# Optimization experiments

Hardware: AMD Instinct MI355X
Metric: run time of the kernel (lower is better)

## Reference

```python
import jax, jax.numpy as jnp
import numpy as np

EPS = 1e-12

def squash(s):
    # standard capsule squash: ||s||^2/(1+||s||^2) * s/||s||
    n2 = jnp.sum(s * s, axis=-1, keepdims=True)
    return n2 / (1.0 + n2) * s / jnp.sqrt(n2 + EPS)

def setup_inputs() -> dict:
    key = jax.random.key(0)
    k1, k2 = jax.random.split(key)
    B, O, I, DOUT, DIN = 64, 32, 2048, 16, 16
    u = jax.random.normal(k1, (B, I, DIN), dtype=jnp.float32)
    # TruncatedNormal(stddev=0.1) init for W
    W = 0.1 * jax.random.truncated_normal(k2, -2.0, 2.0, (1, O, I, DOUT, DIN), dtype=jnp.float32)
    bias = jnp.full((1, O, DOUT), 0.1, dtype=jnp.float32)
    return {"u": u, "W": W, "bias": bias}

def reference(u, W, bias):
    routing_iterations = 3
    O = W.shape[1]
    # u: [B, I, DIN], W: [1, O, I, DOUT, DIN]
    u_norm = jnp.linalg.norm(u, axis=-1)                     # [B, I]
    # u_hat[b,o,i,d] = sum_k W[0,o,i,d,k] * u[b,i,k]  (batched matmul instead of tile+mul+sum)
    u_hat = jnp.einsum('oidk,bik->boid', W[0], u)            # [B, O, I, DOUT]
    u_hat_norm = jnp.linalg.norm(u_hat, axis=-1, keepdims=True)   # [B, O, I, 1]
    new_u_hat_norm = jnp.minimum(u_hat_norm, u_norm[:, None, :, None])
    u_hat = u_hat / (u_hat_norm + EPS) * new_u_hat_norm

    B = u.shape[0]
    b_ij = jnp.zeros((B, O, u.shape[1], 1), dtype=u.dtype)
    t_const = jnp.float32(np.log(0.9 * (O - 1)) - np.log(1.0 - 0.9))
    v_j = None
    c_ij = None
    for r in range(routing_iterations):
        c_ij = jax.nn.softmax(b_ij, axis=1)                  # softmax over out capsules
        s_j = jnp.sum(c_ij * u_hat, axis=2) + bias           # [B, O, DOUT]
        v_j = squash(s_j)
        if r < routing_iterations - 1:
            # gamma-routing agreement: distance between prediction and output
            d = jnp.linalg.norm(v_j[:, :, None, :] - u_hat, axis=-1, keepdims=True)  # [B,O,I,1]
            d_o = jnp.mean(d)
            d_p = d_o * 0.5
            t = t_const / (d_p - d_o + 1e-12)
            b_ij = t * d
    return (v_j, c_ij)
```

## Files before the change

### kernel.cpp

```cpp
#include <hip/hip_runtime.h>
#include <hip/hip_bf16.h>
#include <math.h>

#define BB 64
#define OO 32
#define II 2048
#define DD 16
#define CAPS_EPS 1e-12f
#define T_CONST 5.6312118f

#define GX 128
#define TI 16

#define OFF_DSUM 0ULL
#define OFF_V     16ULL
#define OFF_UNORM 32784ULL
#define OFF_UBF   163856ULL
#define OFF_WB    1212432ULL
#define OFF_DD    9601040ULL
#define OFF_CB    13795344ULL
#define OFF_PART  17989648ULL

typedef __attribute__((ext_vector_type(8))) short bf16x8;
typedef __attribute__((ext_vector_type(4))) float f32x4;

union AU { bf16x8 v; unsigned short h[8]; uint4 u4; };

__device__ __forceinline__ unsigned short f2bf(float x) {
    __hip_bfloat16 h = __float2bfloat16(x);
    unsigned short s; __builtin_memcpy(&s, &h, 2); return s;
}

__global__ __launch_bounds__(256) void uprep_kernel(
    const float* __restrict__ u, float* __restrict__ ws)
{
    const int gid = blockIdx.x * 256 + threadIdx.x;
    if (gid < 2) ws[OFF_DSUM + gid] = 0.f;
    const int i = gid >> 6, b = gid & 63;

    const float4* up = reinterpret_cast<const float4*>(u + ((size_t)b * II + i) * DD);
    float4 t0 = up[0], t1 = up[1], t2 = up[2], t3 = up[3];
    float un2 = t0.x*t0.x + t0.y*t0.y + t0.z*t0.z + t0.w*t0.w
              + t1.x*t1.x + t1.y*t1.y + t1.z*t1.z + t1.w*t1.w
              + t2.x*t2.x + t2.y*t2.y + t2.z*t2.z + t2.w*t2.w
              + t3.x*t3.x + t3.y*t3.y + t3.z*t3.z + t3.w*t3.w;
    ws[OFF_UNORM + (size_t)i * 64 + b] = sqrtf(un2);

    AU a0, a1;
    a0.h[0]=f2bf(t0.x); a0.h[1]=f2bf(t0.y); a0.h[2]=f2bf(t0.z); a0.h[3]=f2bf(t0.w);
    a0.h[4]=f2bf(t1.x); a0.h[5]=f2bf(t1.y); a0.h[6]=f2bf(t1.z); a0.h[7]=f2bf(t1.w);
    a1.h[0]=f2bf(t2.x); a1.h[1]=f2bf(t2.y); a1.h[2]=f2bf(t2.z); a1.h[3]=f2bf(t2.w);
    a1.h[4]=f2bf(t3.x); a1.h[5]=f2bf(t3.y); a1.h[6]=f2bf(t3.z); a1.h[7]=f2bf(t3.w);
    unsigned short* ubf = (unsigned short*)(ws + OFF_UBF);
    uint4* dst = reinterpret_cast<uint4*>(ubf + ((size_t)i * 64 + b) * 16);
    dst[0] = a0.u4; dst[1] = a1.u4;
}

__global__ __launch_bounds__(256) void s0w_kernel(
    const float* __restrict__ W, float* __restrict__ ws)
{
    const int og   = blockIdx.y;
    const int wave = threadIdx.x >> 6;
    const int lane = threadIdx.x & 63;
    const int o    = og * 4 + wave;
    const int q    = lane >> 4;
    const int n    = lane & 15;

    unsigned short* Wb = (unsigned short*)(ws + OFF_WB);
    const unsigned short* ubf = (const unsigned short*)(ws + OFF_UBF);
    const float* unorm = ws + OFF_UNORM;
    float* part = ws + OFF_PART;

    f32x4 s_acc[4];
    #pragma unroll
    for (int g = 0; g < 4; ++g) s_acc[g] = (f32x4){0.f, 0.f, 0.f, 0.f};

    for (int ii = 0; ii < TI; ++ii) {
        const int i = blockIdx.x * TI + ii;

        AU au; au.u4 = make_uint4(0, 0, 0, 0);
        if (q < 2) {
            const float* wp = W + (((size_t)o * II + i) * 16 + n) * 16 + q * 8;
            float4 w0 = *(const float4*)(wp);
            float4 w1 = *(const float4*)(wp + 4);
            au.h[0]=f2bf(w0.x); au.h[1]=f2bf(w0.y); au.h[2]=f2bf(w0.z); au.h[3]=f2bf(w0.w);
            au.h[4]=f2bf(w1.x); au.h[5]=f2bf(w1.y); au.h[6]=f2bf(w1.z); au.h[7]=f2bf(w1.w);
            *reinterpret_cast<uint4*>(Wb + (((size_t)o * II + i) * 2 + q) * 128 + n * 8) = au.u4;
        }

        f32x4 d4[4];
        #pragma unroll
        for (int g = 0; g < 4; ++g) {
            AU bu;
            bu.u4 = *reinterpret_cast<const uint4*>(
                ubf + ((size_t)i * 64 + g * 16 + n) * 16 + (q & 1) * 8);
            d4[g] = __builtin_amdgcn_mfma_f32_16x16x32_bf16(
                au.v, bu.v, (f32x4){0.f, 0.f, 0.f, 0.f}, 0, 0, 0);
        }

        #pragma unroll
        for (int g = 0; g < 4; ++g) {
            float n2 = d4[g][0]*d4[g][0] + d4[g][1]*d4[g][1]
                     + d4[g][2]*d4[g][2] + d4[g][3]*d4[g][3];
            n2 += __shfl_xor(n2, 16);
            n2 += __shfl_xor(n2, 32);
            const float rawn = sqrtf(n2);
            const float un = unorm[(size_t)i * 64 + g * 16 + n];
            const float cs = (1.0f / 32.0f) * fminf(rawn, un) / (rawn + CAPS_EPS);
            s_acc[g][0] += cs * d4[g][0];
            s_acc[g][1] += cs * d4[g][1];
            s_acc[g][2] += cs * d4[g][2];
            s_acc[g][3] += cs * d4[g][3];
        }
    }

    #pragma unroll
    for (int g = 0; g < 4; ++g) {
        float4 v = make_float4(s_acc[g][0], s_acc[g][1], s_acc[g][2], s_acc[g][3]);
        *reinterpret_cast<float4*>(
            part + (((size_t)blockIdx.x * OO + o) * 64 + g * 16 + n) * 16 + q * 4) = v;
    }
}

template<int SLOT>
__global__ __launch_bounds__(256) void dpass_kernel(float* __restrict__ ws)
{
    const int og   = blockIdx.y;
    const int wave = threadIdx.x >> 6;
    const int lane = threadIdx.x & 63;
    const int o    = og * 4 + wave;
    const int q    = lane >> 4;
    const int n    = lane & 15;

    const unsigned short* Wb  = (const unsigned short*)(ws + OFF_WB);
    const unsigned short* ubf = (const unsigned short*)(ws + OFF_UBF);
    const float* unorm = ws + OFF_UNORM;
    const float* v_ws  = ws + OFF_V;
    float* dws = ws + OFF_DD;

    f32x4 vreg[4];
    #pragma unroll
    for (int g = 0; g < 4; ++g)
        vreg[g] = *reinterpret_cast<const f32x4*>(
            v_ws + ((size_t)(g * 16 + n) * OO + o) * 16 + q * 4);

    float dsum_local = 0.f;

    for (int ii = 0; ii < TI; ++ii) {
        const int i = blockIdx.x * TI + ii;

        AU au; au.u4 = make_uint4(0, 0, 0, 0);
        if (q < 2)
            au.u4 = *reinterpret_cast<const uint4*>(
                Wb + (((size_t)o * II + i) * 2 + q) * 128 + n * 8);

        f32x4 d4[4];
        #pragma unroll
        for (int g = 0; g < 4; ++g) {
            AU bu;
            bu.u4 = *reinterpret_cast<const uint4*>(
                ubf + ((size_t)i * 64 + g * 16 + n) * 16 + (q & 1) * 8);
            d4[g] = __builtin_amdgcn_mfma_f32_16x16x32_bf16(
                au.v, bu.v, (f32x4){0.f, 0.f, 0.f, 0.f}, 0, 0, 0);
        }

        #pragma unroll
        for (int g = 0; g < 4; ++g) {
            float n2 = d4[g][0]*d4[g][0] + d4[g][1]*d4[g][1]
                     + d4[g][2]*d4[g][2] + d4[g][3]*d4[g][3];
            n2 += __shfl_xor(n2, 16);
            n2 += __shfl_xor(n2, 32);
            const float rawn = sqrtf(n2);
            const float un = unorm[(size_t)i * 64 + g * 16 + n];
            const float scale = fminf(rawn, un) / (rawn + CAPS_EPS);
            float dd2 = 0.f;
            #pragma unroll
            for (int r = 0; r < 4; ++r) {
                float df = vreg[g][r] - scale * d4[g][r];
                dd2 += df * df;
            }
            dd2 += __shfl_xor(dd2, 16);
            dd2 += __shfl_xor(dd2, 32);
            const float dist = sqrtf(dd2);
            if (q == 0)
                dws[((size_t)i * OO + o) * 64 + g * 16 + n] = dist;
            dsum_local += (q == 0) ? dist : 0.f;
        }
    }

    #pragma unroll
    for (int off = 32; off > 0; off >>= 1)
        dsum_local += __shfl_down(dsum_local, off);
    __shared__ float red[4];
    if (lane == 0) red[wave] = dsum_local;
    __syncthreads();
    if (threadIdx.x == 0)
        atomicAdd(&ws[OFF_DSUM + SLOT], red[0] + red[1] + red[2] + red[3]);
}

template<int SLOT>
__global__ __launch_bounds__(256) void csoft_kernel(float* __restrict__ ws)
{
    const int wave = threadIdx.x >> 6;
    const int b    = threadIdx.x & 63;
    const int i    = blockIdx.x * 4 + wave;

    const float* dws = ws + OFF_DD;
    float* cb = ws + OFF_CB;
    const float dsum = ws[OFF_DSUM + SLOT];
    const float tval = T_CONST / (-0.5f * dsum * (1.0f / 4194304.0f) + 1e-12f);

    float dv[OO];
    #pragma unroll
    for (int o = 0; o < OO; ++o)
        dv[o] = tval * dws[((size_t)i * OO + o) * 64 + b];
    float m = -1e30f;
    #pragma unroll
    for (int o = 0; o < OO; ++o) m = fmaxf(m, dv[o]);
    float ssum = 0.f;
    #pragma unroll
    for (int o = 0; o < OO; ++o) { dv[o] = __expf(dv[o] - m); ssum += dv[o]; }
    const float inv = 1.f / ssum;
    #pragma unroll
    for (int o = 0; o < OO; ++o)
        cb[((size_t)i * OO + o) * 64 + b] = dv[o] * inv;
}

__global__ __launch_bounds__(256) void spass_kernel(float* __restrict__ ws)
{
    const int og   = blockIdx.y;
    const int wave = threadIdx.x >> 6;
    const int lane = threadIdx.x & 63;
    const int o    = og * 4 + wave;
    const int q    = lane >> 4;
    const int n    = lane & 15;

    const unsigned short* Wb  = (const unsigned short*)(ws + OFF_WB);
    const unsigned short* ubf = (const unsigned short*)(ws + OFF_UBF);
    const float* unorm = ws + OFF_UNORM;
    const float* cb = ws + OFF_CB;
    float* part = ws + OFF_PART;

    f32x4 s_acc[4];
    #pragma unroll
    for (int g = 0; g < 4; ++g) s_acc[g] = (f32x4){0.f, 0.f, 0.f, 0.f};

    for (int ii = 0; ii < TI; ++ii) {
        const int i = blockIdx.x * TI + ii;

        AU au; au.u4 = make_uint4(0, 0, 0, 0);
        if (q < 2)
            au.u4 = *reinterpret_cast<const uint4*>(
                Wb + (((size_t)o * II + i) * 2 + q) * 128 + n * 8);

        f32x4 d4[4];
        #pragma unroll
        for (int g = 0; g < 4; ++g) {
            AU bu;
            bu.u4 = *reinterpret_cast<const uint4*>(
                ubf + ((size_t)i * 64 + g * 16 + n) * 16 + (q & 1) * 8);
            d4[g] = __builtin_amdgcn_mfma_f32_16x16x32_bf16(
                au.v, bu.v, (f32x4){0.f, 0.f, 0.f, 0.f}, 0, 0, 0);
        }

        #pragma unroll
        for (int g = 0; g < 4; ++g) {
            float n2 = d4[g][0]*d4[g][0] + d4[g][1]*d4[g][1]
                     + d4[g][2]*d4[g][2] + d4[g][3]*d4[g][3];
            n2 += __shfl_xor(n2, 16);
            n2 += __shfl_xor(n2, 32);
            const float rawn = sqrtf(n2);
            const float un = unorm[(size_t)i * 64 + g * 16 + n];
            const float cc = cb[((size_t)i * OO + o) * 64 + g * 16 + n];
            const float cs = cc * fminf(rawn, un) / (rawn + CAPS_EPS);
            s_acc[g][0] += cs * d4[g][0];
            s_acc[g][1] += cs * d4[g][1];
            s_acc[g][2] += cs * d4[g][2];
            s_acc[g][3] += cs * d4[g][3];
        }
    }

    #pragma unroll
    for (int g = 0; g < 4; ++g) {
        float4 v = make_float4(s_acc[g][0], s_acc[g][1], s_acc[g][2], s_acc[g][3]);
        *reinterpret_cast<float4*>(
            part + (((size_t)blockIdx.x * OO + o) * 64 + g * 16 + n) * 16 + q * 4) = v;
    }
}

__global__ __launch_bounds__(256) void finv_kernel(
    const float* __restrict__ part, const float* __restrict__ bias,
    float* __restrict__ vout)
{
    const int tid = blockIdx.x * 256 + threadIdx.x;
    const int b = tid >> 9, o = (tid >> 4) & 31, d = tid & 15;
    float s = 0.f;
    for (int ic = 0; ic < GX; ++ic)
        s += part[(((size_t)ic * OO + o) * 64 + b) * 16 + d];
    s += bias[tid & 511];
    float n2 = s * s;
    #pragma unroll
    for (int off = 1; off < 16; off <<= 1) n2 += __shfl_xor(n2, off);
    vout[tid] = s * (n2 / (1.f + n2)) * rsqrtf(n2 + CAPS_EPS);
}

__global__ __launch_bounds__(256) void transpose_kernel(
    const float* __restrict__ cb, float* __restrict__ dst)
{
    __shared__ float tile[32][65];
    const int o  = blockIdx.y;
    const int i0 = blockIdx.x * 32;
    #pragma unroll
    for (int k = 0; k < 8; ++k) {
        const int lin = k * 256 + threadIdx.x;
        const int r = lin >> 6, b = lin & 63;
        tile[r][b] = cb[((size_t)(i0 + r) * OO + o) * 64 + b];
    }
    __syncthreads();
    #pragma unroll
    for (int k = 0; k < 8; ++k) {
        const int lin = k * 256 + threadIdx.x;
        const int b = lin >> 5, r = lin & 31;
        dst[((size_t)b * OO + o) * II + i0 + r] = tile[r][b];
    }
}

extern "C" void kernel_launch(void* const* d_in, const int* in_sizes, int n_in,
                              void* d_out, int out_size, void* d_ws, size_t ws_size,
                              hipStream_t stream) {
    const float* u    = (const float*)d_in[0];
    const float* W    = (const float*)d_in[1];
    const float* bias = (const float*)d_in[2];
    float* out = (float*)d_out;
    float* ws  = (float*)d_ws;

    float* part = ws + OFF_PART;
    float* v_ws = ws + OFF_V;
    float* cb   = ws + OFF_CB;
    float* cout = out + (size_t)BB * OO * DD;

    dim3 blk(256);
    dim3 grid_m(GX, 8);

    uprep_kernel<<<512, blk, 0, stream>>>(u, ws);
    s0w_kernel<<<grid_m, blk, 0, stream>>>(W, ws);
    finv_kernel<<<128, blk, 0, stream>>>(part, bias, v_ws);
    dpass_kernel<0><<<grid_m, blk, 0, stream>>>(ws);
    csoft_kernel<0><<<512, blk, 0, stream>>>(ws);
    spass_kernel<<<grid_m, blk, 0, stream>>>(ws);
    finv_kernel<<<128, blk, 0, stream>>>(part, bias, v_ws);
    dpass_kernel<1><<<grid_m, blk, 0, stream>>>(ws);
    csoft_kernel<1><<<512, blk, 0, stream>>>(ws);
    spass_kernel<<<grid_m, blk, 0, stream>>>(ws);
    finv_kernel<<<128, blk, 0, stream>>>(part, bias, out);
    transpose_kernel<<<dim3(64, 32), blk, 0, stream>>>(cb, cout);
}
```

Measured before the change: 332.8 us.

## Cache per-capsule scale and norm, expand distance algebraically, split batch across blocks

The first pass now stores the per-(i,o,b) rescale factor and squared clipped norm to workspace. The distance and s-passes reuse these instead of recomputing the norm, sqrt and division each time. Distance is computed as |v|^2 + |uhat|^2 - 2*scale*(v·uhat) with a clamp at zero, and the y-grid is doubled so each block handles half the batch groups, which adds parallelism. Fast rcp/rsq/sqrt intrinsics replace divisions, at the cost of extra workspace traffic (two new 16 MB arrays) and possible cancellation error in the expanded distance.

```diff
diff --git a/kernel.cpp b/kernel.cpp
--- a/kernel.cpp
+++ b/kernel.cpp
@@ -20,6 +20,8 @@
 #define OFF_DD    9601040ULL
 #define OFF_CB    13795344ULL
 #define OFF_PART  17989648ULL
+#define OFF_SCALE 22183952ULL
+#define OFF_NN2   26378256ULL
 
 typedef __attribute__((ext_vector_type(8))) short bf16x8;
 typedef __attribute__((ext_vector_type(4))) float f32x4;
@@ -44,7 +46,7 @@
               + t1.x*t1.x + t1.y*t1.y + t1.z*t1.z + t1.w*t1.w
               + t2.x*t2.x + t2.y*t2.y + t2.z*t2.z + t2.w*t2.w
               + t3.x*t3.x + t3.y*t3.y + t3.z*t3.z + t3.w*t3.w;
-    ws[OFF_UNORM + (size_t)i * 64 + b] = sqrtf(un2);
+    ws[OFF_UNORM + (size_t)i * 64 + b] = __builtin_amdgcn_sqrtf(un2);
 
     AU a0, a1;
     a0.h[0]=f2bf(t0.x); a0.h[1]=f2bf(t0.y); a0.h[2]=f2bf(t0.z); a0.h[3]=f2bf(t0.w);
@@ -70,6 +72,8 @@
     const unsigned short* ubf = (const unsigned short*)(ws + OFF_UBF);
     const float* unorm = ws + OFF_UNORM;
     float* part = ws + OFF_PART;
+    float* scl  = ws + OFF_SCALE;
+    float* nn2w = ws + OFF_NN2;
 
     f32x4 s_acc[4];
     #pragma unroll
@@ -104,9 +108,17 @@
                      + d4[g][2]*d4[g][2] + d4[g][3]*d4[g][3];
             n2 += __shfl_xor(n2, 16);
             n2 += __shfl_xor(n2, 32);
-            const float rawn = sqrtf(n2);
+            const float rsq  = __builtin_amdgcn_rsqf(n2 + CAPS_EPS);
+            const float rawn = n2 * rsq;
             const float un = unorm[(size_t)i * 64 + g * 16 + n];
-            const float cs = (1.0f / 32.0f) * fminf(rawn, un) / (rawn + CAPS_EPS);
+            const float nn = fminf(rawn, un);
+            const float scale = nn * rsq;
+            if (q == 0) {
+                const size_t idx = ((size_t)i * OO + o) * 64 + g * 16 + n;
+                scl[idx]  = scale;
+                nn2w[idx] = nn * nn;
+            }
+            const float cs = 0.03125f * scale;
             s_acc[g][0] += cs * d4[g][0];
             s_acc[g][1] += cs * d4[g][1];
             s_acc[g][2] += cs * d4[g][2];
@@ -125,7 +137,8 @@
 template<int SLOT>
 __global__ __launch_bounds__(256) void dpass_kernel(float* __restrict__ ws)
 {
-    const int og   = blockIdx.y;
+    const int og   = blockIdx.y >> 1;
+    const int bh   = blockIdx.y & 1;
     const int wave = threadIdx.x >> 6;
     const int lane = threadIdx.x & 63;
     const int o    = og * 4 + wave;
@@ -134,15 +147,24 @@
 
     const unsigned short* Wb  = (const unsigned short*)(ws + OFF_WB);
     const unsigned short* ubf = (const unsigned short*)(ws + OFF_UBF);
-    const float* unorm = ws + OFF_UNORM;
-    const float* v_ws  = ws + OFF_V;
+    const float* v_ws = ws + OFF_V;
+    const float* scl  = ws + OFF_SCALE;
+    const float* nn2w = ws + OFF_NN2;
     float* dws = ws + OFF_DD;
 
-    f32x4 vreg[4];
-    #pragma unroll
-    for (int g = 0; g < 4; ++g)
-        vreg[g] = *reinterpret_cast<const f32x4*>(
+    f32x4 vreg[2];
+    float vn2[2];
+    #pragma unroll
+    for (int gg = 0; gg < 2; ++gg) {
+        const int g = bh * 2 + gg;
+        vreg[gg] = *reinterpret_cast<const f32x4*>(
             v_ws + ((size_t)(g * 16 + n) * OO + o) * 16 + q * 4);
+        float t = vreg[gg][0]*vreg[gg][0] + vreg[gg][1]*vreg[gg][1]
+                + vreg[gg][2]*vreg[gg][2] + vreg[gg][3]*vreg[gg][3];
+        t += __shfl_xor(t, 16);
+        t += __shfl_xor(t, 32);
+        vn2[gg] = t;
+    }
 
     float dsum_local = 0.f;
 
@@ -154,37 +176,28 @@
             au.u4 = *reinterpret_cast<const uint4*>(
                 Wb + (((size_t)o * II + i) * 2 + q) * 128 + n * 8);
 
-        f32x4 d4[4];
         #pragma unroll
-        for (int g = 0; g < 4; ++g) {
+        for (int gg = 0; gg < 2; ++gg) {
+            const int g = bh * 2 + gg;
             AU bu;
             bu.u4 = *reinterpret_cast<const uint4*>(
                 ubf + ((size_t)i * 64 + g * 16 + n) * 16 + (q & 1) * 8);
-            d4[g] = __builtin_amdgcn_mfma_f32_16x16x32_bf16(
+            f32x4 d4 = __builtin_amdgcn_mfma_f32_16x16x32_bf16(
                 au.v, bu.v, (f32x4){0.f, 0.f, 0.f, 0.f}, 0, 0, 0);
-        }
-
-        #pragma unroll
-        for (int g = 0; g < 4; ++g) {
-            float n2 = d4[g][0]*d4[g][0] + d4[g][1]*d4[g][1]
-                     + d4[g][2]*d4[g][2] + d4[g][3]*d4[g][3];
-            n2 += __shfl_xor(n2, 16);
-            n2 += __shfl_xor(n2, 32);
-            const float rawn = sqrtf(n2);
-            const float un = unorm[(size_t)i * 64 + g * 16 + n];
-            const float scale = fminf(rawn, un) / (rawn + CAPS_EPS);
-            float dd2 = 0.f;
-            #pragma unroll
-            for (int r = 0; r < 4; ++r) {
-                float df = vreg[g][r] - scale * d4[g][r];
-                dd2 += df * df;
+
+            float pp = vreg[gg][0]*d4[0] + vreg[gg][1]*d4[1]
+                     + vreg[gg][2]*d4[2] + vreg[gg][3]*d4[3];
+            pp += __shfl_xor(pp, 16);
+            pp += __shfl_xor(pp, 32);
+
+            const size_t idx = ((size_t)i * OO + o) * 64 + g * 16 + n;
+            const float sc  = scl[idx];
+            const float dd2 = fmaxf(vn2[gg] + nn2w[idx] - 2.f * sc * pp, 0.f);
+            const float dist = __builtin_amdgcn_sqrtf(dd2);
+            if (q == 0) {
+                dws[idx] = dist;
+                dsum_local += dist;
             }
-            dd2 += __shfl_xor(dd2, 16);
-            dd2 += __shfl_xor(dd2, 32);
-            const float dist = sqrtf(dd2);
-            if (q == 0)
-                dws[((size_t)i * OO + o) * 64 + g * 16 + n] = dist;
-            dsum_local += (q == 0) ? dist : 0.f;
         }
     }
 
@@ -208,7 +221,8 @@
     const float* dws = ws + OFF_DD;
     float* cb = ws + OFF_CB;
     const float dsum = ws[OFF_DSUM + SLOT];
-    const float tval = T_CONST / (-0.5f * dsum * (1.0f / 4194304.0f) + 1e-12f);
+    const float tval = T_CONST * __builtin_amdgcn_rcpf(
+        -0.5f * dsum * (1.0f / 4194304.0f) + 1e-12f);
 
     float dv[OO];
     #pragma unroll
@@ -220,7 +234,7 @@
     float ssum = 0.f;
     #pragma unroll
     for (int o = 0; o < OO; ++o) { dv[o] = __expf(dv[o] - m); ssum += dv[o]; }
-    const float inv = 1.f / ssum;
+    const float inv = __builtin_amdgcn_rcpf(ssum);
     #pragma unroll
     for (int o = 0; o < OO; ++o)
         cb[((size_t)i * OO + o) * 64 + b] = dv[o] * inv;
@@ -228,7 +242,8 @@
 
 __global__ __launch_bounds__(256) void spass_kernel(float* __restrict__ ws)
 {
-    const int og   = blockIdx.y;
+    const int og   = blockIdx.y >> 1;
+    const int bh   = blockIdx.y & 1;
     const int wave = threadIdx.x >> 6;
     const int lane = threadIdx.x & 63;
     const int o    = og * 4 + wave;
@@ -237,13 +252,13 @@
 
     const unsigned short* Wb  = (const unsigned short*)(ws + OFF_WB);
     const unsigned short* ubf = (const unsigned short*)(ws + OFF_UBF);
-    const float* unorm = ws + OFF_UNORM;
-    const float* cb = ws + OFF_CB;
+    const float* cb  = ws + OFF_CB;
+    const float* scl = ws + OFF_SCALE;
     float* part = ws + OFF_PART;
 
-    f32x4 s_acc[4];
-    #pragma unroll
-    for (int g = 0; g < 4; ++g) s_acc[g] = (f32x4){0.f, 0.f, 0.f, 0.f};
+    f32x4 s_acc[2];
+    #pragma unroll
+    for (int gg = 0; gg < 2; ++gg) s_acc[gg] = (f32x4){0.f, 0.f, 0.f, 0.f};
 
     for (int ii = 0; ii < TI; ++ii) {
         const int i = blockIdx.x * TI + ii;
@@ -253,36 +268,28 @@
             au.u4 = *reinterpret_cast<const uint4*>(
                 Wb + (((size_t)o * II + i) * 2 + q) * 128 + n * 8);
 
-        f32x4 d4[4];
         #pragma unroll
-        for (int g = 0; g < 4; ++g) {
+        for (int gg = 0; gg < 2; ++gg) {
+            const int g = bh * 2 + gg;
             AU bu;
             bu.u4 = *reinterpret_cast<const uint4*>(
                 ubf + ((size_t)i * 64 + g * 16 + n) * 16 + (q & 1) * 8);
-            d4[g] = __builtin_amdgcn_mfma_f32_16x16x32_bf16(
+            f32x4 d4 = __builtin_amdgcn_mfma_f32_16x16x32_bf16(
                 au.v, bu.v, (f32x4){0.f, 0.f, 0.f, 0.f}, 0, 0, 0);
-        }
-
-        #pragma unroll
-        for (int g = 0; g < 4; ++g) {
-            float n2 = d4[g][0]*d4[g][0] + d4[g][1]*d4[g][1]
-                     + d4[g][2]*d4[g][2] + d4[g][3]*d4[g][3];
-            n2 += __shfl_xor(n2, 16);
-            n2 += __shfl_xor(n2, 32);
-            const float rawn = sqrtf(n2);
-            const float un = unorm[(size_t)i * 64 + g * 16 + n];
-            const float cc = cb[((size_t)i * OO + o) * 64 + g * 16 + n];
-            const float cs = cc * fminf(rawn, un) / (rawn + CAPS_EPS);
-            s_acc[g][0] += cs * d4[g][0];
-            s_acc[g][1] += cs * d4[g][1];
-            s_acc[g][2] += cs * d4[g][2];
-            s_acc[g][3] += cs * d4[g][3];
-        }
-    }
-
-    #pragma unroll
-    for (int g = 0; g < 4; ++g) {
-        float4 v = make_float4(s_acc[g][0], s_acc[g][1], s_acc[g][2], s_acc[g][3]);
+
+            const size_t idx = ((size_t)i * OO + o) * 64 + g * 16 + n;
+            const float cs = cb[idx] * scl[idx];
+            s_acc[gg][0] += cs * d4[0];
+            s_acc[gg][1] += cs * d4[1];
+            s_acc[gg][2] += cs * d4[2];
+            s_acc[gg][3] += cs * d4[3];
+        }
+    }
+
+    #pragma unroll
+    for (int gg = 0; gg < 2; ++gg) {
+        const int g = bh * 2 + gg;
+        float4 v = make_float4(s_acc[gg][0], s_acc[gg][1], s_acc[gg][2], s_acc[gg][3]);
         *reinterpret_cast<float4*>(
             part + (((size_t)blockIdx.x * OO + o) * 64 + g * 16 + n) * 16 + q * 4) = v;
     }
@@ -293,15 +300,16 @@
     float* __restrict__ vout)
 {
     const int tid = blockIdx.x * 256 + threadIdx.x;
-    const int b = tid >> 9, o = (tid >> 4) & 31, d = tid & 15;
     float s = 0.f;
+    #pragma unroll 4
     for (int ic = 0; ic < GX; ++ic)
-        s += part[(((size_t)ic * OO + o) * 64 + b) * 16 + d];
+        s += part[(size_t)ic * (OO * 64 * 16) + (tid >> 9) * 16 + ((tid >> 4) & 31) * 1024 + (tid & 15)];
     s += bias[tid & 511];
     float n2 = s * s;
     #pragma unroll
     for (int off = 1; off < 16; off <<= 1) n2 += __shfl_xor(n2, off);
-    vout[tid] = s * (n2 / (1.f + n2)) * rsqrtf(n2 + CAPS_EPS);
+    vout[tid] = s * n2 * __builtin_amdgcn_rcpf(1.f + n2)
+                  * __builtin_amdgcn_rsqf(n2 + CAPS_EPS);
 }
 
 __global__ __launch_bounds__(256) void transpose_kernel(
@@ -341,17 +349,18 @@
 
     dim3 blk(256);
     dim3 grid_m(GX, 8);
+    dim3 grid_d(GX, 16);
 
     uprep_kernel<<<512, blk, 0, stream>>>(u, ws);
     s0w_kernel<<<grid_m, blk, 0, stream>>>(W, ws);
     finv_kernel<<<128, blk, 0, stream>>>(part, bias, v_ws);
-    dpass_kernel<0><<<grid_m, blk, 0, stream>>>(ws);
+    dpass_kernel<0><<<grid_d, blk, 0, stream>>>(ws);
     csoft_kernel<0><<<512, blk, 0, stream>>>(ws);
-    spass_kernel<<<grid_m, blk, 0, stream>>>(ws);
+    spass_kernel<<<grid_d, blk, 0, stream>>>(ws);
     finv_kernel<<<128, blk, 0, stream>>>(part, bias, v_ws);
-    dpass_kernel<1><<<grid_m, blk, 0, stream>>>(ws);
+    dpass_kernel<1><<<grid_d, blk, 0, stream>>>(ws);
     csoft_kernel<1><<<512, blk, 0, stream>>>(ws);
-    spass_kernel<<<grid_m, blk, 0, stream>>>(ws);
+    spass_kernel<<<grid_d, blk, 0, stream>>>(ws);
     finv_kernel<<<128, blk, 0, stream>>>(part, bias, out);
     transpose_kernel<<<dim3(64, 32), blk, 0, stream>>>(cb, cout);
 }
```

New measurement: 353.2 us. 1.06x slower.
